# Kernel optimization log

Hardware: AMD Instinct MI355X
Metric: run time of the kernel (lower is better)

The kernel has to match this reference:

```python
import jax, jax.numpy as jnp
import numpy as np

N, W, T = 8, 64, 8192      # batch, emb_width, time
K_BINS = 2048

def setup_inputs() -> dict:
    key = jax.random.key(0)
    kx, kk = jax.random.split(key)
    x = jax.random.normal(kx, (N, W, T), dtype=jnp.float32)
    k = jax.random.normal(kk, (K_BINS, W), dtype=jnp.float32)
    return {"x": x, "k": k}

def reference(x, k):
    n, w, t = x.shape
    # preprocess: (N, W, T) -> (N*T, W)
    xf = jnp.transpose(x, (0, 2, 1)).reshape(-1, w)
    prenorm = jnp.linalg.norm(xf - jnp.mean(xf)) / np.sqrt(float(xf.size))
    # quantise: squared-euclidean distances via matmul expansion
    # dist[i, j] = ||xf_i||^2 - 2 xf_i . k_j + ||k_j||^2   -> (N*T, K_BINS)
    dist = (jnp.sum(xf * xf, axis=-1, keepdims=True)
            - 2.0 * (xf @ k.T)
            + jnp.sum(k * k, axis=-1)[None, :])
    x_l = jnp.argmin(dist, axis=-1)            # (N*T,)
    fit = jnp.mean(jnp.min(dist, axis=-1))
    # dequantise: embedding gather
    x_d = k[x_l]                               # (N*T, W)
    commit_loss = jnp.sum((jax.lax.stop_gradient(x_d) - xf) ** 2) / float(xf.size)
    # straight-through estimator
    x_d = xf + jax.lax.stop_gradient(x_d - xf)
    # postprocess
    x_l = x_l.reshape(n, t)
    x_d = jnp.transpose(x_d.reshape(n, t, w), (0, 2, 1))  # (N, W, T)
    return x_l, x_d, commit_loss, fit, prenorm
```

## Files before the change

### kernel.cpp

```cpp
#include <hip/hip_runtime.h>
#include <hip/hip_bf16.h>
#include <math.h>

#define N_BATCH 8
#define WDIM 64
#define TDIM 8192
#define KBINS 2048
#define NROWS (N_BATCH * TDIM)
#define XSIZE (N_BATCH * WDIM * TDIM)
#define XL_OFF 0
#define XD_OFF NROWS
#define SCAL_OFF (NROWS + XSIZE)

#define MT 64
#define XST 72
#define TAU 0.05f
#define MAXFLAG 8192
#define NBLK (NROWS / MT)

#define WS_K2_OFF   0
#define WS_CNT_OFF  8192
#define WS_FLAG_OFF 8256
#define WS_SLOT_OFF 41024
#define WS_PART_OFF 106560
#define WS_KF_OFF   122944
#define WS_KT_OFF   647296
#define WS_KT_END   (WS_KT_OFF + (size_t)WDIM * KBINS * 4)

typedef __attribute__((ext_vector_type(8))) short bf16x8;
typedef __attribute__((ext_vector_type(4))) float f32x4;
typedef unsigned long long u64;

static __device__ __forceinline__ short f2bf(float v) {
  __hip_bfloat16 b = __float2bfloat16(v);
  return *reinterpret_cast<short*>(&b);
}
static __device__ __forceinline__ float bf2f(short s) {
  unsigned int u = ((unsigned int)(unsigned short)s) << 16;
  return __uint_as_float(u);
}

#define GLOAD_LDS(gsrc, ldst)                                            \
  __builtin_amdgcn_global_load_lds(                                      \
      (const __attribute__((address_space(1))) unsigned int*)(gsrc),     \
      (__attribute__((address_space(3))) unsigned int*)(ldst), 16, 0, 0)

#define WAIT_VM4 0x0F74
#define WAIT_VM0 0x0F70

#define SBAR() asm volatile("s_barrier" ::: "memory")

__global__ void prep_kernel(const float* __restrict__ kg, float* __restrict__ k2,
                            char* __restrict__ kfrag, float* __restrict__ kT,
                            int* __restrict__ cnt, u64* __restrict__ slots) {
  __shared__ float skc[16 * 65];
  const int tid  = threadIdx.x;
  const int tile = blockIdx.x;
  const int c0   = tile * 16;
  if (tile == 0 && tid == 0) *cnt = 0;
  if (tid < 64) slots[tile * 64 + tid] = ~0ULL;
  {
    const float4* g4 = (const float4*)(kg + (size_t)c0 * WDIM);
    int code = tid >> 4, w = (tid & 15) * 4;
    *(float4*)&skc[code * 65 + w] = g4[tid];
  }
  __syncthreads();
  if (tid < 16) {
    const float* kr = &skc[tid * 65];
    float r[8];
#pragma unroll
    for (int l = 0; l < 8; ++l) r[l] = __fmul_rn(kr[l], kr[l]);
    for (int i = 8; i < WDIM; i += 8) {
#pragma unroll
      for (int l = 0; l < 8; ++l)
        r[l] = __fadd_rn(r[l], __fmul_rn(kr[i + l], kr[i + l]));
    }
    k2[c0 + tid] = __fadd_rn(__fadd_rn(__fadd_rn(r[0], r[1]), __fadd_rn(r[2], r[3])),
                             __fadd_rn(__fadd_rn(r[4], r[5]), __fadd_rn(r[6], r[7])));
  }
  if (kT) {
    const int code = tid & 15;
#pragma unroll
    for (int j = 0; j < 4; ++j) {
      int w = (tid >> 4) + 16 * j;
      kT[(size_t)w * KBINS + c0 + code] = skc[code * 65 + w];
    }
  }
  {
    const int sub  = tid >> 6;
    const int lane = tid & 63;
    const int lcol = lane & 15;
    const int quad = lane >> 4;
    const float* src = &skc[lcol * 65 + (sub & 1) * 32 + quad * 8];
    const bool lo = (sub >= 2);
    short tmp[8];
#pragma unroll
    for (int i = 0; i < 8; ++i) {
      float v = src[i];
      short h = f2bf(v);
      tmp[i] = lo ? f2bf(v - bf2f(h)) : h;
    }
    char* dst = kfrag + (size_t)tile * 4096 + sub * 1024 + lane * 16;
    *(bf16x8*)dst = *(const bf16x8*)tmp;
  }
}

__launch_bounds__(256, 4)
__global__ void vq_mfma(const float* __restrict__ x,
                        const float* __restrict__ kg,
                        const float* __restrict__ k2g,
                        const char* __restrict__ kfrag,
                        float* __restrict__ out,
                        float* __restrict__ part,
                        int* __restrict__ flag_cnt,
                        int* __restrict__ flags) {
  __shared__ __align__(16) char smem[20480];
  char*  kbuf = smem;
  float* k2f  = (float*)(smem + 12288);
  short* sxh = (short*)smem;
  short* sxl = (short*)(smem + 9216);
  float* kd  = (float*)smem;
  int*   sIdx      = (int*)  (smem + 18432);
  float* sPair     = (float*)(smem + 18688);
  int*   sFlagCnt  = (int*)  (smem + 18752);
  int*   sFlagBase = (int*)  (smem + 18756);
  int*   sFlagList = (int*)  (smem + 18760);

  const int tid  = threadIdx.x;
  const int blk  = blockIdx.x;
  const int row0 = blk * MT;
  const int n    = row0 >> 13;
  const int t0   = row0 & (TDIM - 1);

  const int r  = tid & 63;
  const int wh = tid >> 6;
  float x2p = 0.f, sxp = 0.f;
  const float* xb = x + (size_t)n * WDIM * TDIM + t0 + r;
#pragma unroll 8
  for (int i = 0; i < 16; ++i) {
    int w = 4 * i + wh;
    float v = xb[(size_t)w * TDIM];
    x2p = fmaf(v, v, x2p);
    sxp += v;
    short h = f2bf(v);
    sxh[r * XST + w] = h;
    sxl[r * XST + w] = f2bf(v - bf2f(h));
  }
  __syncthreads();

  const int wave = tid >> 6;
  const int lane = tid & 63;
  const int lcol = lane & 15;
  const int quad = lane >> 4;
  const int rA = wave * 16 + lcol;
  bf16x8 ah0 = *(const bf16x8*)&sxh[rA * XST + 0  + quad * 8];
  bf16x8 ah1 = *(const bf16x8*)&sxh[rA * XST + 32 + quad * 8];
  bf16x8 al0 = *(const bf16x8*)&sxl[rA * XST + 0  + quad * 8];
  bf16x8 al1 = *(const bf16x8*)&sxl[rA * XST + 32 + quad * 8];
  __syncthreads();

  float bd[4], b2[4];
  int   bi[4];
#pragma unroll
  for (int i = 0; i < 4; ++i) { bd[i] = 3.0e38f; b2[i] = 3.0e38f; bi[i] = 0; }

  const char* kfg = kfrag;

#define VQ_ISSUE(C, B)                                                       \
  if ((C) < 128) {                                                           \
    const char* s = kfg + (size_t)(C) * 4096 + (lane << 4);                  \
    char* d = kbuf + (B) * 4096;                                             \
    GLOAD_LDS(s, d);                                                         \
    GLOAD_LDS(s + 1024, d + 1024);                                           \
    GLOAD_LDS(s + 2048, d + 2048);                                           \
    GLOAD_LDS(s + 3072, d + 3072);                                           \
  }

  if (wave == 0) {
    VQ_ISSUE(0, 0)
    VQ_ISSUE(1, 1)
  }
  {
    const float4* k24 = (const float4*)k2g;
    *(float4*)&k2f[tid * 8]     = k24[tid * 2];
    *(float4*)&k2f[tid * 8 + 4] = k24[tid * 2 + 1];
  }
  asm volatile("s_waitcnt lgkmcnt(0)\n\ts_barrier" ::: "memory");

#define VQ_STEP(C, RB, PB, WAITIMM)                                          \
  {                                                                          \
    if (wave == 0) __builtin_amdgcn_s_waitcnt(WAITIMM);                      \
    SBAR();                                                                  \
    const char* tb = kbuf + (RB) * 4096;                                     \
    bf16x8 bh0 = *(const bf16x8*)(tb + 0    + (lane << 4));                  \
    bf16x8 bh1 = *(const bf16x8*)(tb + 1024 + (lane << 4));                  \
    bf16x8 bl0 = *(const bf16x8*)(tb + 2048 + (lane << 4));                  \
    bf16x8 bl1 = *(const bf16x8*)(tb + 3072 + (lane << 4));                  \
    float k2c = k2f[(C) * 16 + lcol];                                        \
    if (wave == 0) { VQ_ISSUE((C) + 2, PB) }                                 \
    f32x4 p = {0.f, 0.f, 0.f, 0.f};                                          \
    p = __builtin_amdgcn_mfma_f32_16x16x32_bf16(ah0, bh0, p, 0, 0, 0);       \
    p = __builtin_amdgcn_mfma_f32_16x16x32_bf16(ah1, bh1, p, 0, 0, 0);       \
    p = __builtin_amdgcn_mfma_f32_16x16x32_bf16(ah0, bl0, p, 0, 0, 0);       \
    p = __builtin_amdgcn_mfma_f32_16x16x32_bf16(ah1, bl1, p, 0, 0, 0);       \
    p = __builtin_amdgcn_mfma_f32_16x16x32_bf16(al0, bh0, p, 0, 0, 0);       \
    p = __builtin_amdgcn_mfma_f32_16x16x32_bf16(al1, bh1, p, 0, 0, 0);       \
    const int code = (C) * 16 + lcol;                                        \
    _Pragma("unroll")                                                        \
    for (int i = 0; i < 4; ++i) {                                            \
      float d0 = fmaf(-2.f, p[i], k2c);                                      \
      float nb2 = __builtin_amdgcn_fmed3f(bd[i], d0, b2[i]);                 \
      bool lt0 = d0 < bd[i];                                                 \
      bd[i] = lt0 ? d0 : bd[i];                                              \
      bi[i] = lt0 ? code : bi[i];                                            \
      b2[i] = nb2;                                                           \
    }                                                                        \
  }

  for (int c = 0; c < 126; c += 3) {
    VQ_STEP(c,     0, 2, WAIT_VM4)
    VQ_STEP(c + 1, 1, 0, WAIT_VM4)
    VQ_STEP(c + 2, 2, 1, WAIT_VM4)
  }
  VQ_STEP(126, 0, 2, WAIT_VM4)
  VQ_STEP(127, 1, 0, WAIT_VM0)
#undef VQ_STEP
#undef VQ_ISSUE

#pragma unroll
  for (int m = 1; m < 16; m <<= 1) {
#pragma unroll
    for (int i = 0; i < 4; ++i) {
      float od  = __shfl_xor(bd[i], m, 64);
      float od2 = __shfl_xor(b2[i], m, 64);
      int   oi  = __shfl_xor(bi[i], m, 64);
      float nb2 = fminf(fminf(b2[i], od2), fmaxf(bd[i], od));
      bool take = (od < bd[i]) || (od == bd[i] && oi < bi[i]);
      bd[i] = take ? od : bd[i];
      bi[i] = take ? oi : bi[i];
      b2[i] = nb2;
    }
  }

  __syncthreads();
  if (tid == 0) *sFlagCnt = 0;
  __syncthreads();

  float fit_p = 0.f;
  if (lcol == 0) {
#pragma unroll
    for (int i = 0; i < 4; ++i) {
      int rloc = wave * 16 + quad * 4 + i;
      int rowg = row0 + rloc;
      out[XL_OFF + rowg] = (float)bi[i];
      sIdx[rloc] = bi[i];
      fit_p += bd[i];
      if (b2[i] - bd[i] < TAU) {
        int slot = atomicAdd(sFlagCnt, 1);
        sFlagList[slot] = rowg;
      }
    }
  }
  __syncthreads();

  int nloc = *sFlagCnt;
  if (tid == 0 && nloc > 0) *sFlagBase = atomicAdd(flag_cnt, nloc);
  __syncthreads();
  if (tid < nloc) {
    int gs = *sFlagBase + tid;
    if (gs < MAXFLAG) flags[gs] = sFlagList[tid];
  }

  {
    int rr = tid >> 2, q4 = tid & 3;
    const float4* kr4 = (const float4*)(kg + (size_t)sIdx[rr] * WDIM) + q4 * 4;
    float4* dst = (float4*)&kd[rr * 68 + q4 * 16];
#pragma unroll
    for (int j = 0; j < 4; ++j) dst[j] = kr4[j];
  }
  __syncthreads();

  float commit_p = 0.f;
  float* xdb = out + XD_OFF + (size_t)n * WDIM * TDIM + t0 + r;
#pragma unroll 8
  for (int i = 0; i < 16; ++i) {
    int w = 4 * i + wh;
    float xvv = xb[(size_t)w * TDIM];
    float kvv = kd[r * 68 + w];
    float df = kvv - xvv;
    commit_p = fmaf(df, df, commit_p);
    xdb[(size_t)w * TDIM] = kvv;
  }

  float v0 = sxp, v1 = x2p, v2 = commit_p, v3 = fit_p;
#pragma unroll
  for (int off = 32; off > 0; off >>= 1) {
    v0 += __shfl_down(v0, off, 64);
    v1 += __shfl_down(v1, off, 64);
    v2 += __shfl_down(v2, off, 64);
    v3 += __shfl_down(v3, off, 64);
  }
  if (lane == 0) {
    sPair[wave * 4 + 0] = v0;
    sPair[wave * 4 + 1] = v1;
    sPair[wave * 4 + 2] = v2;
    sPair[wave * 4 + 3] = v3;
  }
  __syncthreads();
  if (tid == 0) {
    float x2sum = sPair[1] + sPair[5] + sPair[9] + sPair[13];
    part[0 * NBLK + blk] = sPair[0] + sPair[4] + sPair[8] + sPair[12];
    part[1 * NBLK + blk] = x2sum;
    part[2 * NBLK + blk] = sPair[2] + sPair[6] + sPair[10] + sPair[14];
    part[3 * NBLK + blk] = (sPair[3] + sPair[7] + sPair[11] + sPair[15]) + x2sum;
  }
}

__launch_bounds__(256, 4)
__global__ void recheck_scan(const float* __restrict__ x,
                             const float* __restrict__ kg,
                             const float* __restrict__ kT,
                             const float* __restrict__ k2g,
                             const int* __restrict__ flag_cnt,
                             const int* __restrict__ flags,
                             u64* __restrict__ slots) {
  __shared__ float sx[WDIM];
  __shared__ float sx2s;
  const int tid = threadIdx.x;
  int nf = *flag_cnt;
  if (nf > MAXFLAG) nf = MAXFLAG;
  const int total = nf * 8;

  for (int g = blockIdx.x; g < total; g += 2048) {
    const int fi  = g >> 3;
    const int seg = g & 7;
    const int row = flags[fi];
    const int n = row >> 13;
    const int t = row & (TDIM - 1);
    if (tid < WDIM) sx[tid] = x[(size_t)n * WDIM * TDIM + (size_t)tid * TDIM + t];
    __syncthreads();
    if (tid == 0) {
      float r8[8];
#pragma unroll
      for (int l = 0; l < 8; ++l) r8[l] = __fmul_rn(sx[l], sx[l]);
      for (int i = 8; i < WDIM; i += 8) {
#pragma unroll
        for (int l = 0; l < 8; ++l)
          r8[l] = __fadd_rn(r8[l], __fmul_rn(sx[i + l], sx[i + l]));
      }
      sx2s = __fadd_rn(__fadd_rn(__fadd_rn(r8[0], r8[1]), __fadd_rn(r8[2], r8[3])),
                       __fadd_rn(__fadd_rn(r8[4], r8[5]), __fadd_rn(r8[6], r8[7])));
    }
    __syncthreads();

    const int j = seg * 256 + tid;
    float c = 0.f;
    if (kT) {
#pragma unroll
      for (int w = 0; w < WDIM; ++w)
        c = __fmaf_rn(sx[w], kT[(size_t)w * KBINS + j], c);
    } else {
      const float* kr = kg + (size_t)j * WDIM;
#pragma unroll
      for (int w = 0; w < WDIM; ++w)
        c = __fmaf_rn(sx[w], kr[w], c);
    }
    float d = __fadd_rn(__fsub_rn(sx2s, __fmul_rn(2.0f, c)), k2g[j]);

    u64 key = ((u64)__float_as_uint(d) << 32) | (unsigned int)j;
#pragma unroll
    for (int off = 32; off > 0; off >>= 1) {
      u64 o = __shfl_down((unsigned long long)key, off, 64);
      if (o < key) key = o;
    }
    if ((tid & 63) == 0) atomicMin(&slots[fi], key);
    __syncthreads();
  }
}

__global__ void recheck_write(const float* __restrict__ kg,
                              const int* __restrict__ flag_cnt,
                              const int* __restrict__ flags,
                              const u64* __restrict__ slots,
                              float* __restrict__ out) {
  int nf = *flag_cnt;
  if (nf > MAXFLAG) nf = MAXFLAG;
  const int w = threadIdx.x;
  for (int fi = blockIdx.x; fi < nf; fi += 256) {
    const int row = flags[fi];
    const int n = row >> 13;
    const int t = row & (TDIM - 1);
    const int j = (int)(slots[fi] & 0xFFFFFFFFULL);
    if (w == 0) out[XL_OFF + row] = (float)j;
    out[XD_OFF + (size_t)n * WDIM * TDIM + (size_t)w * TDIM + t] = kg[(size_t)j * WDIM + w];
  }
}

__global__ void finalize_kernel(const float* __restrict__ part, float* __restrict__ out) {
  __shared__ double sred[4][64];
  const int tid = threadIdx.x;
  const int lane = tid & 63;
  const int wv = tid >> 6;
  double a[4] = {0.0, 0.0, 0.0, 0.0};
  for (int i = tid; i < NBLK; i += 256) {
#pragma unroll
    for (int q = 0; q < 4; ++q) a[q] += (double)part[q * NBLK + i];
  }
#pragma unroll
  for (int off = 32; off > 0; off >>= 1) {
#pragma unroll
    for (int q = 0; q < 4; ++q)
      a[q] += __shfl_down(a[q], off, 64);
  }
  if (lane == 0) {
#pragma unroll
    for (int q = 0; q < 4; ++q) sred[q][wv] = a[q];
  }
  __syncthreads();
  if (tid == 0) {
    double s0 = 0, s1 = 0, s2 = 0, s3 = 0;
#pragma unroll
    for (int wv2 = 0; wv2 < 4; ++wv2) {
      s0 += sred[0][wv2]; s1 += sred[1][wv2];
      s2 += sred[2][wv2]; s3 += sred[3][wv2];
    }
    double size = (double)XSIZE;
    double commit = s2 / size;
    double fit = s3 / (double)NROWS;
    double mean = s0 / size;
    double var = s1 / size - mean * mean;
    if (var < 0.0) var = 0.0;
    out[SCAL_OFF + 0] = (float)commit;
    out[SCAL_OFF + 1] = (float)fit;
    out[SCAL_OFF + 2] = (float)sqrt(var);
  }
}

extern "C" void kernel_launch(void* const* d_in, const int* in_sizes, int n_in,
                              void* d_out, int out_size, void* d_ws, size_t ws_size,
                              hipStream_t stream) {
  const float* x = (const float*)d_in[0];
  const float* kg = (const float*)d_in[1];
  float* out = (float*)d_out;
  float* k2   = (float*)((char*)d_ws + WS_K2_OFF);
  int* cnt    = (int*)((char*)d_ws + WS_CNT_OFF);
  int* flags  = (int*)((char*)d_ws + WS_FLAG_OFF);
  u64* slots  = (u64*)((char*)d_ws + WS_SLOT_OFF);
  float* part = (float*)((char*)d_ws + WS_PART_OFF);
  char* kfrag = (char*)d_ws + WS_KF_OFF;
  float* kT   = (ws_size >= WS_KT_END) ? (float*)((char*)d_ws + WS_KT_OFF) : nullptr;

  hipLaunchKernelGGL(prep_kernel, dim3(KBINS / 16), dim3(256), 0, stream,
                     kg, k2, kfrag, kT, cnt, slots);
  hipLaunchKernelGGL(vq_mfma, dim3(NBLK), dim3(256), 0, stream,
                     x, kg, k2, kfrag, out, part, cnt, flags);
  hipLaunchKernelGGL(recheck_scan, dim3(2048), dim3(256), 0, stream,
                     x, kg, kT, k2, cnt, flags, slots);
  hipLaunchKernelGGL(recheck_write, dim3(256), dim3(WDIM), 0, stream,
                     kg, cnt, flags, slots, out);
  hipLaunchKernelGGL(finalize_kernel, dim3(1), dim3(256), 0, stream, part, out);
}
```

Baseline: 167.3 us.

## Split codebook scan across two wave teams per block with LDS merge

Doubles the vq_mfma block to 512 threads and splits the 2048-entry codebook into two halves, each scanned by its own team of four waves with a separate triple-buffered LDS ring. Each team handles only 64 codebook tiles, so the serial chain of barrier-separated MFMA steps per block is halved. Team 1 writes its per-row best, second-best and index to LDS, and team 0 merges them before writing outputs and flags. The cost is more LDS per block (about 34 KB), block-wide barriers across 8 waves, and two codebook streams per block instead of one.

New measurement: 263.7 us. 57.6% more time.

```diff
diff --git a/kernel.cpp b/kernel.cpp
--- a/kernel.cpp
+++ b/kernel.cpp
@@ -105,7 +105,7 @@
   }
 }
 
-__launch_bounds__(256, 4)
+__launch_bounds__(512, 8)
 __global__ void vq_mfma(const float* __restrict__ x,
                         const float* __restrict__ kg,
                         const float* __restrict__ k2g,
@@ -114,17 +114,20 @@
                         float* __restrict__ part,
                         int* __restrict__ flag_cnt,
                         int* __restrict__ flags) {
-  __shared__ __align__(16) char smem[20480];
+  __shared__ __align__(16) char smem[34184];
   char*  kbuf = smem;
-  float* k2f  = (float*)(smem + 12288);
+  float* k2f  = (float*)(smem + 24576);
+  float* mbd       = (float*)(smem + 32768);
+  float* mb2       = (float*)(smem + 33024);
+  int*   mbi       = (int*)  (smem + 33280);
+  int*   sIdx      = (int*)  (smem + 33536);
+  float* sPair     = (float*)(smem + 33792);
+  int*   sFlagCnt  = (int*)  (smem + 33920);
+  int*   sFlagBase = (int*)  (smem + 33924);
+  int*   sFlagList = (int*)  (smem + 33928);
   short* sxh = (short*)smem;
   short* sxl = (short*)(smem + 9216);
   float* kd  = (float*)smem;
-  int*   sIdx      = (int*)  (smem + 18432);
-  float* sPair     = (float*)(smem + 18688);
-  int*   sFlagCnt  = (int*)  (smem + 18752);
-  int*   sFlagBase = (int*)  (smem + 18756);
-  int*   sFlagList = (int*)  (smem + 18760);
 
   const int tid  = threadIdx.x;
   const int blk  = blockIdx.x;
@@ -136,9 +139,9 @@
   const int wh = tid >> 6;
   float x2p = 0.f, sxp = 0.f;
   const float* xb = x + (size_t)n * WDIM * TDIM + t0 + r;
-#pragma unroll 8
-  for (int i = 0; i < 16; ++i) {
-    int w = 4 * i + wh;
+#pragma unroll
+  for (int i = 0; i < 8; ++i) {
+    int w = 8 * i + wh;
     float v = xb[(size_t)w * TDIM];
     x2p = fmaf(v, v, x2p);
     sxp += v;
@@ -146,13 +149,20 @@
     sxh[r * XST + w] = h;
     sxl[r * XST + w] = f2bf(v - bf2f(h));
   }
+  {
+    const float4* k24 = (const float4*)k2g;
+    *(float4*)&k2f[tid * 4] = k24[tid];
+  }
   __syncthreads();
 
   const int wave = tid >> 6;
   const int lane = tid & 63;
   const int lcol = lane & 15;
   const int quad = lane >> 4;
-  const int rA = wave * 16 + lcol;
+  const int team = wave >> 2;
+  const int g    = wave & 3;
+  const bool iw  = (g == 0);
+  const int rA = g * 16 + lcol;
   bf16x8 ah0 = *(const bf16x8*)&sxh[rA * XST + 0  + quad * 8];
   bf16x8 ah1 = *(const bf16x8*)&sxh[rA * XST + 32 + quad * 8];
   bf16x8 al0 = *(const bf16x8*)&sxl[rA * XST + 0  + quad * 8];
@@ -165,39 +175,36 @@
   for (int i = 0; i < 4; ++i) { bd[i] = 3.0e38f; b2[i] = 3.0e38f; bi[i] = 0; }
 
   const char* kfg = kfrag;
-
-#define VQ_ISSUE(C, B)                                                       \
-  if ((C) < 128) {                                                           \
-    const char* s = kfg + (size_t)(C) * 4096 + (lane << 4);                  \
-    char* d = kbuf + (B) * 4096;                                             \
+  char* myring = kbuf + team * 12288;
+  const int Tb = team * 64;
+
+#define VQ_ISSUE(CG, B)                                                      \
+  {                                                                          \
+    const char* s = kfg + (size_t)(CG) * 4096 + (lane << 4);                 \
+    char* d = myring + (B) * 4096;                                           \
     GLOAD_LDS(s, d);                                                         \
     GLOAD_LDS(s + 1024, d + 1024);                                           \
     GLOAD_LDS(s + 2048, d + 2048);                                           \
     GLOAD_LDS(s + 3072, d + 3072);                                           \
   }
 
-  if (wave == 0) {
-    VQ_ISSUE(0, 0)
-    VQ_ISSUE(1, 1)
-  }
-  {
-    const float4* k24 = (const float4*)k2g;
-    *(float4*)&k2f[tid * 8]     = k24[tid * 2];
-    *(float4*)&k2f[tid * 8 + 4] = k24[tid * 2 + 1];
-  }
-  asm volatile("s_waitcnt lgkmcnt(0)\n\ts_barrier" ::: "memory");
-
-#define VQ_STEP(C, RB, PB, WAITIMM)                                          \
+  if (iw) {
+    VQ_ISSUE(Tb + 0, 0)
+    VQ_ISSUE(Tb + 1, 1)
+  }
+
+#define VQ_STEP(CR, RB, PB, WAITIMM, DOISS)                                  \
   {                                                                          \
-    if (wave == 0) __builtin_amdgcn_s_waitcnt(WAITIMM);                      \
+    if (iw) __builtin_amdgcn_s_waitcnt(WAITIMM);                             \
     SBAR();                                                                  \
-    const char* tb = kbuf + (RB) * 4096;                                     \
+    const char* tb = myring + (RB) * 4096;                                   \
     bf16x8 bh0 = *(const bf16x8*)(tb + 0    + (lane << 4));                  \
     bf16x8 bh1 = *(const bf16x8*)(tb + 1024 + (lane << 4));                  \
     bf16x8 bl0 = *(const bf16x8*)(tb + 2048 + (lane << 4));                  \
     bf16x8 bl1 = *(const bf16x8*)(tb + 3072 + (lane << 4));                  \
-    float k2c = k2f[(C) * 16 + lcol];                                        \
-    if (wave == 0) { VQ_ISSUE((C) + 2, PB) }                                 \
+    const int cg = Tb + (CR);                                                \
+    float k2c = k2f[cg * 16 + lcol];                                         \
+    if (iw && (DOISS)) { VQ_ISSUE(cg + 2, PB) }                              \
     f32x4 p = {0.f, 0.f, 0.f, 0.f};                                          \
     p = __builtin_amdgcn_mfma_f32_16x16x32_bf16(ah0, bh0, p, 0, 0, 0);       \
     p = __builtin_amdgcn_mfma_f32_16x16x32_bf16(ah1, bh1, p, 0, 0, 0);       \
@@ -205,7 +212,7 @@
     p = __builtin_amdgcn_mfma_f32_16x16x32_bf16(ah1, bl1, p, 0, 0, 0);       \
     p = __builtin_amdgcn_mfma_f32_16x16x32_bf16(al0, bh0, p, 0, 0, 0);       \
     p = __builtin_amdgcn_mfma_f32_16x16x32_bf16(al1, bh1, p, 0, 0, 0);       \
-    const int code = (C) * 16 + lcol;                                        \
+    const int code = cg * 16 + lcol;                                         \
     _Pragma("unroll")                                                        \
     for (int i = 0; i < 4; ++i) {                                            \
       float d0 = fmaf(-2.f, p[i], k2c);                                      \
@@ -217,13 +224,15 @@
     }                                                                        \
   }
 
-  for (int c = 0; c < 126; c += 3) {
-    VQ_STEP(c,     0, 2, WAIT_VM4)
-    VQ_STEP(c + 1, 1, 0, WAIT_VM4)
-    VQ_STEP(c + 2, 2, 1, WAIT_VM4)
-  }
-  VQ_STEP(126, 0, 2, WAIT_VM4)
-  VQ_STEP(127, 1, 0, WAIT_VM0)
+  for (int c = 0; c < 60; c += 3) {
+    VQ_STEP(c,     0, 2, WAIT_VM4, 1)
+    VQ_STEP(c + 1, 1, 0, WAIT_VM4, 1)
+    VQ_STEP(c + 2, 2, 1, WAIT_VM4, 1)
+  }
+  VQ_STEP(60, 0, 2, WAIT_VM4, 1)
+  VQ_STEP(61, 1, 0, WAIT_VM4, 1)
+  VQ_STEP(62, 2, 1, WAIT_VM4, 0)
+  VQ_STEP(63, 0, 2, WAIT_VM0, 0)
 #undef VQ_STEP
 #undef VQ_ISSUE
 
@@ -244,18 +253,33 @@
 
   __syncthreads();
   if (tid == 0) *sFlagCnt = 0;
+  if (team == 1 && lcol == 0) {
+#pragma unroll
+    for (int i = 0; i < 4; ++i) {
+      int rloc = g * 16 + quad * 4 + i;
+      mbd[rloc] = bd[i];
+      mb2[rloc] = b2[i];
+      mbi[rloc] = bi[i];
+    }
+  }
   __syncthreads();
 
   float fit_p = 0.f;
-  if (lcol == 0) {
+  if (team == 0 && lcol == 0) {
 #pragma unroll
     for (int i = 0; i < 4; ++i) {
-      int rloc = wave * 16 + quad * 4 + i;
+      int rloc = g * 16 + quad * 4 + i;
       int rowg = row0 + rloc;
-      out[XL_OFF + rowg] = (float)bi[i];
-      sIdx[rloc] = bi[i];
-      fit_p += bd[i];
-      if (b2[i] - bd[i] < TAU) {
+      float obd = mbd[rloc], ob2 = mb2[rloc];
+      int   obi = mbi[rloc];
+      float nb2 = fminf(fminf(b2[i], ob2), fmaxf(bd[i], obd));
+      bool take = obd < bd[i];
+      float fbd = take ? obd : bd[i];
+      int   fbi = take ? obi : bi[i];
+      out[XL_OFF + rowg] = (float)fbi;
+      sIdx[rloc] = fbi;
+      fit_p += fbd;
+      if (nb2 - fbd < TAU) {
         int slot = atomicAdd(sFlagCnt, 1);
         sFlagList[slot] = rowg;
       }
@@ -272,19 +296,19 @@
   }
 
   {
-    int rr = tid >> 2, q4 = tid & 3;
-    const float4* kr4 = (const float4*)(kg + (size_t)sIdx[rr] * WDIM) + q4 * 4;
-    float4* dst = (float4*)&kd[rr * 68 + q4 * 16];
-#pragma unroll
-    for (int j = 0; j < 4; ++j) dst[j] = kr4[j];
+    int rr = tid >> 3, q8 = tid & 7;
+    const float4* kr4 = (const float4*)(kg + (size_t)sIdx[rr] * WDIM) + q8 * 2;
+    float4* dst = (float4*)&kd[rr * 68 + q8 * 8];
+    dst[0] = kr4[0];
+    dst[1] = kr4[1];
   }
   __syncthreads();
 
   float commit_p = 0.f;
   float* xdb = out + XD_OFF + (size_t)n * WDIM * TDIM + t0 + r;
-#pragma unroll 8
-  for (int i = 0; i < 16; ++i) {
-    int w = 4 * i + wh;
+#pragma unroll
+  for (int i = 0; i < 8; ++i) {
+    int w = 8 * i + wh;
     float xvv = xb[(size_t)w * TDIM];
     float kvv = kd[r * 68 + w];
     float df = kvv - xvv;
@@ -308,11 +332,18 @@
   }
   __syncthreads();
   if (tid == 0) {
-    float x2sum = sPair[1] + sPair[5] + sPair[9] + sPair[13];
-    part[0 * NBLK + blk] = sPair[0] + sPair[4] + sPair[8] + sPair[12];
-    part[1 * NBLK + blk] = x2sum;
-    part[2 * NBLK + blk] = sPair[2] + sPair[6] + sPair[10] + sPair[14];
-    part[3 * NBLK + blk] = (sPair[3] + sPair[7] + sPair[11] + sPair[15]) + x2sum;
+    float s0 = 0.f, s1 = 0.f, s2 = 0.f, s3 = 0.f;
+#pragma unroll
+    for (int w8 = 0; w8 < 8; ++w8) {
+      s0 += sPair[w8 * 4 + 0];
+      s1 += sPair[w8 * 4 + 1];
+      s2 += sPair[w8 * 4 + 2];
+      s3 += sPair[w8 * 4 + 3];
+    }
+    part[0 * NBLK + blk] = s0;
+    part[1 * NBLK + blk] = s1;
+    part[2 * NBLK + blk] = s2;
+    part[3 * NBLK + blk] = s3 + s1;
   }
 }
 
@@ -452,7 +483,7 @@
 
   hipLaunchKernelGGL(prep_kernel, dim3(KBINS / 16), dim3(256), 0, stream,
                      kg, k2, kfrag, kT, cnt, slots);
-  hipLaunchKernelGGL(vq_mfma, dim3(NBLK), dim3(256), 0, stream,
+  hipLaunchKernelGGL(vq_mfma, dim3(NBLK), dim3(512), 0, stream,
                      x, kg, k2, kfrag, out, part, cnt, flags);
   hipLaunchKernelGGL(recheck_scan, dim3(2048), dim3(256), 0, stream,
                      x, kg, kT, k2, cnt, flags, slots);
```

## Process two code tiles per pipeline step and restructure flagged-row rescan

Applied to the files above, without the earlier changes.

The main VQ kernel now loads two 16-code tiles (8 KB) per pipeline stage and runs two independent MFMA accumulation chains interleaved. This halves the number of barriers and wait points per code and gives the MFMA units more independent work. LDS use grows to about 33 KB, which may limit occupancy. The recheck scan now gives each block a whole flagged row and loops over all 8 code segments. It reduces within the block before issuing one atomicMin, instead of splitting each row across 8 blocks.

After: 256.7 us. 53.5% more time.

```diff
diff --git a/kernel.cpp b/kernel.cpp
--- a/kernel.cpp
+++ b/kernel.cpp
@@ -45,9 +45,8 @@
       (const __attribute__((address_space(1))) unsigned int*)(gsrc),     \
       (__attribute__((address_space(3))) unsigned int*)(ldst), 16, 0, 0)
 
-#define WAIT_VM4 0x0F74
+#define WAIT_VM8 0x0F78
 #define WAIT_VM0 0x0F70
-
 #define SBAR() asm volatile("s_barrier" ::: "memory")
 
 __global__ void prep_kernel(const float* __restrict__ kg, float* __restrict__ k2,
@@ -106,7 +105,7 @@
 }
 
 __launch_bounds__(256, 4)
-__global__ void vq_mfma(const float* __restrict__ x,
+__global__ void vq_mono(const float* __restrict__ x,
                         const float* __restrict__ kg,
                         const float* __restrict__ k2g,
                         const char* __restrict__ kfrag,
@@ -114,17 +113,17 @@
                         float* __restrict__ part,
                         int* __restrict__ flag_cnt,
                         int* __restrict__ flags) {
-  __shared__ __align__(16) char smem[20480];
+  __shared__ __align__(16) char smem[33408];
   char*  kbuf = smem;
-  float* k2f  = (float*)(smem + 12288);
+  float* k2f  = (float*)(smem + 24576);
+  int*   sIdx      = (int*)  (smem + 32768);
+  float* sPair     = (float*)(smem + 33024);
+  int*   sFlagCnt  = (int*)  (smem + 33088);
+  int*   sFlagBase = (int*)  (smem + 33092);
+  int*   sFlagList = (int*)  (smem + 33096);
   short* sxh = (short*)smem;
   short* sxl = (short*)(smem + 9216);
   float* kd  = (float*)smem;
-  int*   sIdx      = (int*)  (smem + 18432);
-  float* sPair     = (float*)(smem + 18688);
-  int*   sFlagCnt  = (int*)  (smem + 18752);
-  int*   sFlagBase = (int*)  (smem + 18756);
-  int*   sFlagList = (int*)  (smem + 18760);
 
   const int tid  = threadIdx.x;
   const int blk  = blockIdx.x;
@@ -146,6 +145,11 @@
     sxh[r * XST + w] = h;
     sxl[r * XST + w] = f2bf(v - bf2f(h));
   }
+  {
+    const float4* k24 = (const float4*)k2g;
+    *(float4*)&k2f[tid * 8]     = k24[tid * 2];
+    *(float4*)&k2f[tid * 8 + 4] = k24[tid * 2 + 1];
+  }
   __syncthreads();
 
   const int wave = tid >> 6;
@@ -166,66 +170,84 @@
 
   const char* kfg = kfrag;
 
-#define VQ_ISSUE(C, B)                                                       \
-  if ((C) < 128) {                                                           \
+#define VQ_ISSUE2(C, P)                                                      \
+  {                                                                          \
     const char* s = kfg + (size_t)(C) * 4096 + (lane << 4);                  \
-    char* d = kbuf + (B) * 4096;                                             \
+    char* d = kbuf + (P) * 8192;                                             \
     GLOAD_LDS(s, d);                                                         \
     GLOAD_LDS(s + 1024, d + 1024);                                           \
     GLOAD_LDS(s + 2048, d + 2048);                                           \
     GLOAD_LDS(s + 3072, d + 3072);                                           \
+    GLOAD_LDS(s + 4096, d + 4096);                                           \
+    GLOAD_LDS(s + 5120, d + 5120);                                           \
+    GLOAD_LDS(s + 6144, d + 6144);                                           \
+    GLOAD_LDS(s + 7168, d + 7168);                                           \
   }
 
   if (wave == 0) {
-    VQ_ISSUE(0, 0)
-    VQ_ISSUE(1, 1)
-  }
-  {
-    const float4* k24 = (const float4*)k2g;
-    *(float4*)&k2f[tid * 8]     = k24[tid * 2];
-    *(float4*)&k2f[tid * 8 + 4] = k24[tid * 2 + 1];
-  }
-  asm volatile("s_waitcnt lgkmcnt(0)\n\ts_barrier" ::: "memory");
-
-#define VQ_STEP(C, RB, PB, WAITIMM)                                          \
+    VQ_ISSUE2(0, 0)
+    VQ_ISSUE2(2, 1)
+  }
+
+#define VQ_STEP2(C, P, IP, WAITIMM, DOISS)                                   \
   {                                                                          \
     if (wave == 0) __builtin_amdgcn_s_waitcnt(WAITIMM);                      \
     SBAR();                                                                  \
-    const char* tb = kbuf + (RB) * 4096;                                     \
-    bf16x8 bh0 = *(const bf16x8*)(tb + 0    + (lane << 4));                  \
-    bf16x8 bh1 = *(const bf16x8*)(tb + 1024 + (lane << 4));                  \
-    bf16x8 bl0 = *(const bf16x8*)(tb + 2048 + (lane << 4));                  \
-    bf16x8 bl1 = *(const bf16x8*)(tb + 3072 + (lane << 4));                  \
-    float k2c = k2f[(C) * 16 + lcol];                                        \
-    if (wave == 0) { VQ_ISSUE((C) + 2, PB) }                                 \
+    const char* ta = kbuf + (P) * 8192;                                      \
+    bf16x8 xh0 = *(const bf16x8*)(ta + 0    + (lane << 4));                  \
+    bf16x8 xh1 = *(const bf16x8*)(ta + 1024 + (lane << 4));                  \
+    bf16x8 xl0 = *(const bf16x8*)(ta + 2048 + (lane << 4));                  \
+    bf16x8 xl1 = *(const bf16x8*)(ta + 3072 + (lane << 4));                  \
+    bf16x8 yh0 = *(const bf16x8*)(ta + 4096 + (lane << 4));                  \
+    bf16x8 yh1 = *(const bf16x8*)(ta + 5120 + (lane << 4));                  \
+    bf16x8 yl0 = *(const bf16x8*)(ta + 6144 + (lane << 4));                  \
+    bf16x8 yl1 = *(const bf16x8*)(ta + 7168 + (lane << 4));                  \
+    float k2a = k2f[(C) * 16 + lcol];                                        \
+    float k2b = k2f[(C) * 16 + 16 + lcol];                                   \
+    if (wave == 0 && (DOISS)) { VQ_ISSUE2((C) + 4, IP) }                     \
     f32x4 p = {0.f, 0.f, 0.f, 0.f};                                          \
-    p = __builtin_amdgcn_mfma_f32_16x16x32_bf16(ah0, bh0, p, 0, 0, 0);       \
-    p = __builtin_amdgcn_mfma_f32_16x16x32_bf16(ah1, bh1, p, 0, 0, 0);       \
-    p = __builtin_amdgcn_mfma_f32_16x16x32_bf16(ah0, bl0, p, 0, 0, 0);       \
-    p = __builtin_amdgcn_mfma_f32_16x16x32_bf16(ah1, bl1, p, 0, 0, 0);       \
-    p = __builtin_amdgcn_mfma_f32_16x16x32_bf16(al0, bh0, p, 0, 0, 0);       \
-    p = __builtin_amdgcn_mfma_f32_16x16x32_bf16(al1, bh1, p, 0, 0, 0);       \
-    const int code = (C) * 16 + lcol;                                        \
+    f32x4 q = {0.f, 0.f, 0.f, 0.f};                                          \
+    p = __builtin_amdgcn_mfma_f32_16x16x32_bf16(ah0, xh0, p, 0, 0, 0);       \
+    q = __builtin_amdgcn_mfma_f32_16x16x32_bf16(ah0, yh0, q, 0, 0, 0);       \
+    p = __builtin_amdgcn_mfma_f32_16x16x32_bf16(ah1, xh1, p, 0, 0, 0);       \
+    q = __builtin_amdgcn_mfma_f32_16x16x32_bf16(ah1, yh1, q, 0, 0, 0);       \
+    p = __builtin_amdgcn_mfma_f32_16x16x32_bf16(ah0, xl0, p, 0, 0, 0);       \
+    q = __builtin_amdgcn_mfma_f32_16x16x32_bf16(ah0, yl0, q, 0, 0, 0);       \
+    p = __builtin_amdgcn_mfma_f32_16x16x32_bf16(ah1, xl1, p, 0, 0, 0);       \
+    q = __builtin_amdgcn_mfma_f32_16x16x32_bf16(ah1, yl1, q, 0, 0, 0);       \
+    p = __builtin_amdgcn_mfma_f32_16x16x32_bf16(al0, xh0, p, 0, 0, 0);       \
+    q = __builtin_amdgcn_mfma_f32_16x16x32_bf16(al0, yh0, q, 0, 0, 0);       \
+    p = __builtin_amdgcn_mfma_f32_16x16x32_bf16(al1, xh1, p, 0, 0, 0);       \
+    q = __builtin_amdgcn_mfma_f32_16x16x32_bf16(al1, yh1, q, 0, 0, 0);       \
+    const int codeA = (C) * 16 + lcol;                                       \
     _Pragma("unroll")                                                        \
     for (int i = 0; i < 4; ++i) {                                            \
-      float d0 = fmaf(-2.f, p[i], k2c);                                      \
+      float d0 = fmaf(-2.f, p[i], k2a);                                      \
       float nb2 = __builtin_amdgcn_fmed3f(bd[i], d0, b2[i]);                 \
       bool lt0 = d0 < bd[i];                                                 \
       bd[i] = lt0 ? d0 : bd[i];                                              \
-      bi[i] = lt0 ? code : bi[i];                                            \
+      bi[i] = lt0 ? codeA : bi[i];                                           \
       b2[i] = nb2;                                                           \
+      float d1 = fmaf(-2.f, q[i], k2b);                                      \
+      float nb2b = __builtin_amdgcn_fmed3f(bd[i], d1, b2[i]);                \
+      bool lt1 = d1 < bd[i];                                                 \
+      bd[i] = lt1 ? d1 : bd[i];                                              \
+      bi[i] = lt1 ? (codeA + 16) : bi[i];                                    \
+      b2[i] = nb2b;                                                          \
     }                                                                        \
   }
 
-  for (int c = 0; c < 126; c += 3) {
-    VQ_STEP(c,     0, 2, WAIT_VM4)
-    VQ_STEP(c + 1, 1, 0, WAIT_VM4)
-    VQ_STEP(c + 2, 2, 1, WAIT_VM4)
-  }
-  VQ_STEP(126, 0, 2, WAIT_VM4)
-  VQ_STEP(127, 1, 0, WAIT_VM0)
-#undef VQ_STEP
-#undef VQ_ISSUE
+  for (int c = 0; c < 120; c += 6) {
+    VQ_STEP2(c,     0, 2, WAIT_VM8, 1)
+    VQ_STEP2(c + 2, 1, 0, WAIT_VM8, 1)
+    VQ_STEP2(c + 4, 2, 1, WAIT_VM8, 1)
+  }
+  VQ_STEP2(120, 0, 2, WAIT_VM8, 1)
+  VQ_STEP2(122, 1, 0, WAIT_VM8, 1)
+  VQ_STEP2(124, 2, 1, WAIT_VM8, 0)
+  VQ_STEP2(126, 0, 2, WAIT_VM0, 0)
+#undef VQ_STEP2
+#undef VQ_ISSUE2
 
 #pragma unroll
   for (int m = 1; m < 16; m <<= 1) {
@@ -326,14 +348,14 @@
                              u64* __restrict__ slots) {
   __shared__ float sx[WDIM];
   __shared__ float sx2s;
-  const int tid = threadIdx.x;
+  __shared__ u64 swm[4];
+  const int tid  = threadIdx.x;
+  const int lane = tid & 63;
+  const int wv   = tid >> 6;
   int nf = *flag_cnt;
   if (nf > MAXFLAG) nf = MAXFLAG;
-  const int total = nf * 8;
-
-  for (int g = blockIdx.x; g < total; g += 2048) {
-    const int fi  = g >> 3;
-    const int seg = g & 7;
+
+  for (int fi = blockIdx.x; fi < nf; fi += 1024) {
     const int row = flags[fi];
     const int n = row >> 13;
     const int t = row & (TDIM - 1);
@@ -353,27 +375,38 @@
     }
     __syncthreads();
 
-    const int j = seg * 256 + tid;
-    float c = 0.f;
-    if (kT) {
-#pragma unroll
-      for (int w = 0; w < WDIM; ++w)
-        c = __fmaf_rn(sx[w], kT[(size_t)w * KBINS + j], c);
-    } else {
-      const float* kr = kg + (size_t)j * WDIM;
-#pragma unroll
-      for (int w = 0; w < WDIM; ++w)
-        c = __fmaf_rn(sx[w], kr[w], c);
-    }
-    float d = __fadd_rn(__fsub_rn(sx2s, __fmul_rn(2.0f, c)), k2g[j]);
-
-    u64 key = ((u64)__float_as_uint(d) << 32) | (unsigned int)j;
+    u64 best = ~0ULL;
+#pragma unroll 1
+    for (int s = 0; s < 8; ++s) {
+      const int j = s * 256 + tid;
+      float c = 0.f;
+      if (kT) {
+#pragma unroll
+        for (int w = 0; w < WDIM; ++w)
+          c = __fmaf_rn(sx[w], kT[(size_t)w * KBINS + j], c);
+      } else {
+        const float* kr = kg + (size_t)j * WDIM;
+#pragma unroll
+        for (int w = 0; w < WDIM; ++w)
+          c = __fmaf_rn(sx[w], kr[w], c);
+      }
+      float d = __fadd_rn(__fsub_rn(sx2s, __fmul_rn(2.0f, c)), k2g[j]);
+      u64 key = ((u64)__float_as_uint(d) << 32) | (unsigned)j;
+      best = (key < best) ? key : best;
+    }
 #pragma unroll
     for (int off = 32; off > 0; off >>= 1) {
-      u64 o = __shfl_down((unsigned long long)key, off, 64);
-      if (o < key) key = o;
-    }
-    if ((tid & 63) == 0) atomicMin(&slots[fi], key);
+      u64 o = __shfl_down((unsigned long long)best, off, 64);
+      if (o < best) best = o;
+    }
+    if (lane == 0) swm[wv] = best;
+    __syncthreads();
+    if (tid == 0) {
+      u64 b = swm[0];
+#pragma unroll
+      for (int k = 1; k < 4; ++k) b = (swm[k] < b) ? swm[k] : b;
+      atomicMin(&slots[fi], b);
+    }
     __syncthreads();
   }
 }
@@ -452,9 +485,9 @@
 
   hipLaunchKernelGGL(prep_kernel, dim3(KBINS / 16), dim3(256), 0, stream,
                      kg, k2, kfrag, kT, cnt, slots);
-  hipLaunchKernelGGL(vq_mfma, dim3(NBLK), dim3(256), 0, stream,
+  hipLaunchKernelGGL(vq_mono, dim3(NBLK), dim3(256), 0, stream,
                      x, kg, k2, kfrag, out, part, cnt, flags);
-  hipLaunchKernelGGL(recheck_scan, dim3(2048), dim3(256), 0, stream,
+  hipLaunchKernelGGL(recheck_scan, dim3(1024), dim3(256), 0, stream,
                      x, kg, kT, k2, cnt, flags, slots);
   hipLaunchKernelGGL(recheck_write, dim3(256), dim3(WDIM), 0, stream,
                      kg, cnt, flags, slots, out);
```

## Batch sixteen flagged rows per block in recheck scan to reuse codebook registers

Applied to the files above, without the earlier changes.

The exact-fp32 recheck kernel now processes 16 flagged rows per block: it loads those rows into shared memory once, keeps each thread's codebook column in 64 registers, and loops over the rows with a block-local atomicMin before one global atomicMin per row. Before, it used one block per (row, 256-code segment) and reloaded codebook data for every flagged row. This is meant to cut codebook memory traffic and per-block launch and sync overhead. In exchange it raises register pressure (launch bounds lowered to 2) and uses fewer blocks. The k2 preload is also moved ahead of the initial async codebook-tile issue, and the main kernel is renamed.

After: 228.4 us. 1.37x slower.

```diff
diff --git a/kernel.cpp b/kernel.cpp
--- a/kernel.cpp
+++ b/kernel.cpp
@@ -17,6 +17,7 @@
 #define TAU 0.05f
 #define MAXFLAG 8192
 #define NBLK (NROWS / MT)
+#define RPB 16
 
 #define WS_K2_OFF   0
 #define WS_CNT_OFF  8192
@@ -47,7 +48,6 @@
 
 #define WAIT_VM4 0x0F74
 #define WAIT_VM0 0x0F70
-
 #define SBAR() asm volatile("s_barrier" ::: "memory")
 
 __global__ void prep_kernel(const float* __restrict__ kg, float* __restrict__ k2,
@@ -106,7 +106,7 @@
 }
 
 __launch_bounds__(256, 4)
-__global__ void vq_mfma(const float* __restrict__ x,
+__global__ void vq_mono(const float* __restrict__ x,
                         const float* __restrict__ kg,
                         const float* __restrict__ k2g,
                         const char* __restrict__ kfrag,
@@ -166,7 +166,7 @@
 
   const char* kfg = kfrag;
 
-#define VQ_ISSUE(C, B)                                                       \
+#define VQM_ISSUE(C, B)                                                      \
   if ((C) < 128) {                                                           \
     const char* s = kfg + (size_t)(C) * 4096 + (lane << 4);                  \
     char* d = kbuf + (B) * 4096;                                             \
@@ -176,18 +176,18 @@
     GLOAD_LDS(s + 3072, d + 3072);                                           \
   }
 
-  if (wave == 0) {
-    VQ_ISSUE(0, 0)
-    VQ_ISSUE(1, 1)
-  }
   {
     const float4* k24 = (const float4*)k2g;
     *(float4*)&k2f[tid * 8]     = k24[tid * 2];
     *(float4*)&k2f[tid * 8 + 4] = k24[tid * 2 + 1];
   }
+  if (wave == 0) {
+    VQM_ISSUE(0, 0)
+    VQM_ISSUE(1, 1)
+  }
   asm volatile("s_waitcnt lgkmcnt(0)\n\ts_barrier" ::: "memory");
 
-#define VQ_STEP(C, RB, PB, WAITIMM)                                          \
+#define VQM_STEP(C, RB, PB, WAITIMM)                                         \
   {                                                                          \
     if (wave == 0) __builtin_amdgcn_s_waitcnt(WAITIMM);                      \
     SBAR();                                                                  \
@@ -197,7 +197,7 @@
     bf16x8 bl0 = *(const bf16x8*)(tb + 2048 + (lane << 4));                  \
     bf16x8 bl1 = *(const bf16x8*)(tb + 3072 + (lane << 4));                  \
     float k2c = k2f[(C) * 16 + lcol];                                        \
-    if (wave == 0) { VQ_ISSUE((C) + 2, PB) }                                 \
+    if (wave == 0) { VQM_ISSUE((C) + 2, PB) }                                \
     f32x4 p = {0.f, 0.f, 0.f, 0.f};                                          \
     p = __builtin_amdgcn_mfma_f32_16x16x32_bf16(ah0, bh0, p, 0, 0, 0);       \
     p = __builtin_amdgcn_mfma_f32_16x16x32_bf16(ah1, bh1, p, 0, 0, 0);       \
@@ -218,14 +218,14 @@
   }
 
   for (int c = 0; c < 126; c += 3) {
-    VQ_STEP(c,     0, 2, WAIT_VM4)
-    VQ_STEP(c + 1, 1, 0, WAIT_VM4)
-    VQ_STEP(c + 2, 2, 1, WAIT_VM4)
-  }
-  VQ_STEP(126, 0, 2, WAIT_VM4)
-  VQ_STEP(127, 1, 0, WAIT_VM0)
-#undef VQ_STEP
-#undef VQ_ISSUE
+    VQM_STEP(c,     0, 2, WAIT_VM4)
+    VQM_STEP(c + 1, 1, 0, WAIT_VM4)
+    VQM_STEP(c + 2, 2, 1, WAIT_VM4)
+  }
+  VQM_STEP(126, 0, 2, WAIT_VM4)
+  VQM_STEP(127, 1, 0, WAIT_VM0)
+#undef VQM_STEP
+#undef VQM_ISSUE
 
 #pragma unroll
   for (int m = 1; m < 16; m <<= 1) {
@@ -316,7 +316,7 @@
   }
 }
 
-__launch_bounds__(256, 4)
+__launch_bounds__(256, 2)
 __global__ void recheck_scan(const float* __restrict__ x,
                              const float* __restrict__ kg,
                              const float* __restrict__ kT,
@@ -324,58 +324,78 @@
                              const int* __restrict__ flag_cnt,
                              const int* __restrict__ flags,
                              u64* __restrict__ slots) {
-  __shared__ float sx[WDIM];
-  __shared__ float sx2s;
+  __shared__ float xr[RPB][68];
+  __shared__ float sx2[RPB];
+  __shared__ u64   bestL[RPB];
   const int tid = threadIdx.x;
   int nf = *flag_cnt;
   if (nf > MAXFLAG) nf = MAXFLAG;
-  const int total = nf * 8;
-
-  for (int g = blockIdx.x; g < total; g += 2048) {
-    const int fi  = g >> 3;
-    const int seg = g & 7;
-    const int row = flags[fi];
-    const int n = row >> 13;
-    const int t = row & (TDIM - 1);
-    if (tid < WDIM) sx[tid] = x[(size_t)n * WDIM * TDIM + (size_t)tid * TDIM + t];
-    __syncthreads();
-    if (tid == 0) {
-      float r8[8];
-#pragma unroll
-      for (int l = 0; l < 8; ++l) r8[l] = __fmul_rn(sx[l], sx[l]);
-      for (int i = 8; i < WDIM; i += 8) {
-#pragma unroll
-        for (int l = 0; l < 8; ++l)
-          r8[l] = __fadd_rn(r8[l], __fmul_rn(sx[i + l], sx[i + l]));
-      }
-      sx2s = __fadd_rn(__fadd_rn(__fadd_rn(r8[0], r8[1]), __fadd_rn(r8[2], r8[3])),
-                       __fadd_rn(__fadd_rn(r8[4], r8[5]), __fadd_rn(r8[6], r8[7])));
-    }
-    __syncthreads();
-
-    const int j = seg * 256 + tid;
-    float c = 0.f;
+  const int fi0 = blockIdx.x * RPB;
+  if (fi0 >= nf) return;
+  const int nr = min(RPB, nf - fi0);
+
+  {
+    int rr = tid >> 4;
+    int wq = (tid & 15) * 4;
+    if (rr < nr) {
+      int row = flags[fi0 + rr];
+      int n = row >> 13, t = row & (TDIM - 1);
+      const float* xp = x + (size_t)n * WDIM * TDIM + t;
+#pragma unroll
+      for (int u = 0; u < 4; ++u)
+        xr[rr][wq + u] = xp[(size_t)(wq + u) * TDIM];
+    } else if (rr < RPB) {
+#pragma unroll
+      for (int u = 0; u < 4; ++u) xr[rr][wq + u] = 0.f;
+    }
+  }
+  if (tid < RPB) bestL[tid] = ~0ULL;
+  __syncthreads();
+  if (tid < RPB) {
+    const float* sxp = xr[tid];
+    float r8[8];
+#pragma unroll
+    for (int l = 0; l < 8; ++l) r8[l] = __fmul_rn(sxp[l], sxp[l]);
+    for (int i = 8; i < WDIM; i += 8) {
+#pragma unroll
+      for (int l = 0; l < 8; ++l)
+        r8[l] = __fadd_rn(r8[l], __fmul_rn(sxp[i + l], sxp[i + l]));
+    }
+    sx2[tid] = __fadd_rn(__fadd_rn(__fadd_rn(r8[0], r8[1]), __fadd_rn(r8[2], r8[3])),
+                         __fadd_rn(__fadd_rn(r8[4], r8[5]), __fadd_rn(r8[6], r8[7])));
+  }
+  __syncthreads();
+
+  for (int j0 = 0; j0 < KBINS; j0 += 256) {
+    const int j = j0 + tid;
+    float kreg[WDIM];
     if (kT) {
 #pragma unroll
-      for (int w = 0; w < WDIM; ++w)
-        c = __fmaf_rn(sx[w], kT[(size_t)w * KBINS + j], c);
+      for (int w = 0; w < WDIM; ++w) kreg[w] = kT[(size_t)w * KBINS + j];
     } else {
       const float* kr = kg + (size_t)j * WDIM;
 #pragma unroll
+      for (int w = 0; w < WDIM; ++w) kreg[w] = kr[w];
+    }
+    const float k2j = k2g[j];
+#pragma unroll 2
+    for (int rr = 0; rr < RPB; ++rr) {
+      float c = 0.f;
+#pragma unroll
       for (int w = 0; w < WDIM; ++w)
-        c = __fmaf_rn(sx[w], kr[w], c);
-    }
-    float d = __fadd_rn(__fsub_rn(sx2s, __fmul_rn(2.0f, c)), k2g[j]);
-
-    u64 key = ((u64)__float_as_uint(d) << 32) | (unsigned int)j;
-#pragma unroll
-    for (int off = 32; off > 0; off >>= 1) {
-      u64 o = __shfl_down((unsigned long long)key, off, 64);
-      if (o < key) key = o;
-    }
-    if ((tid & 63) == 0) atomicMin(&slots[fi], key);
-    __syncthreads();
-  }
+        c = __fmaf_rn(xr[rr][w], kreg[w], c);
+      float d = __fadd_rn(__fsub_rn(sx2[rr], __fmul_rn(2.0f, c)), k2j);
+      u64 key = ((u64)__float_as_uint(d) << 32) | (unsigned)j;
+#pragma unroll
+      for (int off = 32; off > 0; off >>= 1) {
+        u64 o = __shfl_down((unsigned long long)key, off, 64);
+        if (o < key) key = o;
+      }
+      if ((tid & 63) == 0) atomicMin(&bestL[rr], key);
+    }
+  }
+  __syncthreads();
+  if (tid < nr) atomicMin(&slots[fi0 + tid], bestL[tid]);
 }
 
 __global__ void recheck_write(const float* __restrict__ kg,
@@ -452,9 +472,9 @@
 
   hipLaunchKernelGGL(prep_kernel, dim3(KBINS / 16), dim3(256), 0, stream,
                      kg, k2, kfrag, kT, cnt, slots);
-  hipLaunchKernelGGL(vq_mfma, dim3(NBLK), dim3(256), 0, stream,
+  hipLaunchKernelGGL(vq_mono, dim3(NBLK), dim3(256), 0, stream,
                      x, kg, k2, kfrag, out, part, cnt, flags);
-  hipLaunchKernelGGL(recheck_scan, dim3(2048), dim3(256), 0, stream,
+  hipLaunchKernelGGL(recheck_scan, dim3(MAXFLAG / RPB), dim3(256), 0, stream,
                      x, kg, kT, k2, cnt, flags, slots);
   hipLaunchKernelGGL(recheck_write, dim3(256), dim3(WDIM), 0, stream,
                      kg, cnt, flags, slots, out);
```
